# Optimization experiments

Measured on AMD Instinct MI355X. Metric: run time of the kernel, lower is better.

## Reference

```python
import jax, jax.numpy as jnp
import numpy as np

B, T, N, D, H = 16, 12, 325, 64, 4
E = 2600
NEG_SLOPE = 0.2
LN_EPS = 1e-5
SM_EPS = 1e-16


def setup_inputs() -> dict:
    key = jax.random.key(0)
    ks = jax.random.split(key, 8)
    x = jax.random.normal(ks[0], (B, T, N, D), dtype=jnp.float32)
    edge_index = jax.random.randint(ks[1], (2, E), 0, N, dtype=jnp.int64)
    W = jax.random.normal(ks[2], (D, H, D), dtype=jnp.float32) * 0.05   # lin weight, [in, heads, out]
    att_src = jax.random.normal(ks[3], (H, D), dtype=jnp.float32) * 0.05
    att_dst = jax.random.normal(ks[4], (H, D), dtype=jnp.float32) * 0.05
    bias = jnp.zeros((D,), dtype=jnp.float32)
    gamma = jnp.ones((D,), dtype=jnp.float32)
    beta = jnp.zeros((D,), dtype=jnp.float32)
    return {"x": x, "W": W, "att_src": att_src, "att_dst": att_dst,
            "bias": bias, "gamma": gamma, "beta": beta, "edge_index": edge_index}


def reference(x, W, att_src, att_dst, bias, gamma, beta, edge_index):
    b, t, n, d = x.shape
    bt = b * t
    xb = x.reshape(bt, n, d)

    # add self-loops (GATConv default add_self_loops=True)
    loops = jnp.arange(n, dtype=edge_index.dtype)
    src = jnp.concatenate([edge_index[0], loops])  # message source j
    dst = jnp.concatenate([edge_index[1], loops])  # message target i

    # per-head linear projection, node axis leading for segment ops: [N, BT, H, D]
    xp = jnp.einsum('bnd,dhf->nbhf', xb, W)

    a_src = jnp.einsum('nbhf,hf->nbh', xp, att_src)  # [N, BT, H]
    a_dst = jnp.einsum('nbhf,hf->nbh', xp, att_dst)

    alpha = a_src[src] + a_dst[dst]                  # [Etot, BT, H]
    alpha = jnp.where(alpha >= 0, alpha, NEG_SLOPE * alpha)

    # segment softmax over incoming edges of each dst node
    m = jax.ops.segment_max(alpha, dst, num_segments=n)        # [N, BT, H]
    e = jnp.exp(alpha - m[dst])
    s = jax.ops.segment_sum(e, dst, num_segments=n)            # [N, BT, H]
    coef = e / (s[dst] + SM_EPS)                               # [Etot, BT, H]

    # weighted scatter-sum aggregation
    msgs = coef[..., None] * xp[src]                           # [Etot, BT, H, D]
    out = jax.ops.segment_sum(msgs, dst, num_segments=n)       # [N, BT, H, D]

    out = out.mean(axis=2) + bias                              # concat=False -> head mean; [N, BT, D]
    out = out.transpose(1, 0, 2).reshape(b, t, n, d)

    # residual + LayerNorm
    y = x + out
    mu = y.mean(axis=-1, keepdims=True)
    var = y.var(axis=-1, keepdims=True)
    return (y - mu) * jax.lax.rsqrt(var + LN_EPS) * gamma + beta
```

## Files before the change

### kernel.cpp

```cpp
#include <hip/hip_runtime.h>

#define Nn 325
#define Dd 64
#define Hh 4
#define Ee 2600
#define BT 192
#define ETOT (Ee+Nn)
#define NROWS (BT*Nn)
#define XPS 136

#define XP_B   (Nn * XPS * 2)
#define COEF_B (ETOT * 8)
#define SMEM_BYTES (XP_B + COEF_B + 2600 + 2600 + ((Nn + 1) * 4) + (ETOT * 4) + (Nn * 4))

typedef __attribute__((ext_vector_type(8))) short bf16x8;
typedef __attribute__((ext_vector_type(4))) float f32x4;

static __device__ __forceinline__ short f2bf(float f) {
    union { float f; unsigned u; } v; v.f = f;
    unsigned r = v.u + 0x7fffu + ((v.u >> 16) & 1u);
    return (short)(r >> 16);
}
static __device__ __forceinline__ float bf_lo(unsigned p) {
    union { unsigned u; float f; } v; v.u = p << 16; return v.f;
}
static __device__ __forceinline__ float bf_hi(unsigned p) {
    union { unsigned u; float f; } v; v.u = p & 0xffff0000u; return v.f;
}

__global__ __launch_bounds__(256) void k_pre(
    const float* __restrict__ W, unsigned short* __restrict__ Wt,
    const int* __restrict__ ei, int* __restrict__ offs, int* __restrict__ elist,
    int* __restrict__ perm, const float* __restrict__ x,
    unsigned short* __restrict__ xbf)
{
    const int t = threadIdx.x;
    if (blockIdx.x < 64) {
        const int f = blockIdx.x * 256 + t;
        const int thr = f >> 6, idx = f & 63;
        const int ct = idx >> 4, kk = (idx >> 3) & 1, j = idx & 7;
        const int w = thr >> 6, lane = thr & 63;
        const int q = lane >> 4, l16 = lane & 15;
        Wt[f] = (unsigned short)f2bf(
            W[(size_t)(kk * 32 + q * 8 + j) * 256 + w * 64 + ct * 16 + l16]);
        return;
    }
    if (blockIdx.x >= 65) {
        const int bx = blockIdx.x - 65;
        #pragma unroll
        for (int k = 0; k < 8; ++k) {
            const int idx = bx * 2048 + k * 256 + t;
            if (idx < (NROWS * Dd) / 4) {
                float4 v = ((const float4*)x)[idx];
                ushort4 o;
                o.x = (unsigned short)f2bf(v.x);
                o.y = (unsigned short)f2bf(v.y);
                o.z = (unsigned short)f2bf(v.z);
                o.w = (unsigned short)f2bf(v.w);
                ((ushort4*)xbf)[idx] = o;
            }
        }
        return;
    }
    __shared__ int cnt[Nn + 1];
    __shared__ int cur[Nn];
    __shared__ int dh[64];
    __shared__ int startS[64];
    const int lane = t & 63;
    for (int i = t; i <= Nn; i += 256) cnt[i] = 0;
    if (t < 64) dh[t] = 0;
    __syncthreads();
    for (int e = t; e < ETOT; e += 256) {
        int d = (e < Ee) ? ei[Ee + e] : (e - Ee);
        atomicAdd(&cnt[d + 1], 1);
    }
    __syncthreads();
    if (t < 64) {
        int run = 0;
        for (int c = 0; c < 6; ++c) {
            int i = c * 64 + lane;
            int v = (i <= Nn) ? cnt[i] : 0;
            #pragma unroll
            for (int off = 1; off < 64; off <<= 1) {
                int u = __shfl_up(v, off);
                if (lane >= off) v += u;
            }
            v += run;
            if (i <= Nn) cnt[i] = v;
            run = __shfl(v, 63);
        }
    }
    __syncthreads();
    for (int i = t; i <= Nn; i += 256) offs[i] = cnt[i];
    for (int i = t; i < Nn; i += 256) cur[i] = cnt[i];
    for (int n = t; n < Nn; n += 256)
        atomicAdd(&dh[min(cnt[n + 1] - cnt[n], 63)], 1);
    __syncthreads();
    if (t < 64) {
        int v = dh[63 - lane];
        int inc = v;
        #pragma unroll
        for (int off = 1; off < 64; off <<= 1) {
            int u = __shfl_up(inc, off);
            if (lane >= off) inc += u;
        }
        startS[63 - lane] = inc - v;
    }
    __syncthreads();
    for (int e = t; e < ETOT; e += 256) {
        int s, d;
        if (e < Ee) { s = ei[e]; d = ei[Ee + e]; }
        else        { s = e - Ee; d = e - Ee; }
        int slot = atomicAdd(&cur[d], 1);
        elist[slot] = s;
    }
    for (int n = t; n < Nn; n += 256) {
        int slot = atomicAdd(&startS[min(cnt[n + 1] - cnt[n], 63)], 1);
        perm[slot] = n;
    }
}

__global__ __launch_bounds__(1024, 4) void k_fused(
    const float* __restrict__ x, const unsigned short* __restrict__ xbf,
    const unsigned short* __restrict__ Wt,
    const float* __restrict__ att_src, const float* __restrict__ att_dst,
    const int* __restrict__ offs, const int* __restrict__ elist,
    const int* __restrict__ perm,
    const float* __restrict__ bias, const float* __restrict__ gamma,
    const float* __restrict__ beta, float* __restrict__ out)
{
    const int bt   = blockIdx.x;
    const int t    = threadIdx.x;
    const int wv   = t >> 6;
    const int lane = t & 63;
    const int q    = lane >> 4;
    const int l16  = lane & 15;
    const int btN  = bt * Nn;

    extern __shared__ char smem[];
    unsigned short* xpS   = (unsigned short*)smem;
    float2*         coefS = (float2*)(smem + XP_B);
    float*          asrcS = (float*)(smem + XP_B + COEF_B);
    float*          adstS = asrcS + 2 * Nn;
    int*            offsS = (int*)(adstS + 2 * Nn);
    int*            elistS= offsS + (Nn + 1);
    int*            permS = elistS + ETOT;

    for (int i = t; i < ETOT; i += 1024) elistS[i] = elist[i];
    for (int i = t; i <= Nn; i += 1024) offsS[i] = offs[i];
    for (int i = t; i < Nn; i += 1024) permS[i] = perm[i];

    float accO[6][4];
    #pragma unroll
    for (int i = 0; i < 6; ++i)
        accO[i][0] = accO[i][1] = accO[i][2] = accO[i][3] = 0.f;

    const int hh  = wv >> 3;
    const int rtb = wv & 7;
    const int g   = wv * 4 + q;

    #pragma unroll 2
    for (int p = 0; p < 2; ++p) {
        const int h = p * 2 + hh;
        bf16x8 bfr[4][2];
        const bf16x8* wtp = (const bf16x8*)(Wt + (size_t)(h * 64 + lane) * 64);
        #pragma unroll
        for (int ct = 0; ct < 4; ++ct) {
            bfr[ct][0] = wtp[ct * 2];
            bfr[ct][1] = wtp[ct * 2 + 1];
        }
        float avs[4], avd[4];
        #pragma unroll
        for (int ct = 0; ct < 4; ++ct) {
            avs[ct] = att_src[h * 64 + ct * 16 + l16];
            avd[ct] = att_dst[h * 64 + ct * 16 + l16];
        }
        if (p) __syncthreads();

        #pragma unroll
        for (int k3 = 0; k3 < 3; ++k3) {
            const int rt = rtb + 8 * k3;
            if (rt > 20) break;
            const int na = min(rt * 16 + l16, Nn - 1);
            bf16x8 afr[2];
            #pragma unroll
            for (int kk = 0; kk < 2; ++kk)
                afr[kk] = *(const bf16x8*)(xbf + (size_t)(btN + na) * 64 + kk * 32 + q * 8);
            f32x4 acc[4];
            #pragma unroll
            for (int ct = 0; ct < 4; ++ct) {
                acc[ct] = (f32x4){0.f, 0.f, 0.f, 0.f};
                acc[ct] = __builtin_amdgcn_mfma_f32_16x16x32_bf16(afr[0], bfr[ct][0], acc[ct], 0, 0, 0);
                acc[ct] = __builtin_amdgcn_mfma_f32_16x16x32_bf16(afr[1], bfr[ct][1], acc[ct], 0, 0, 0);
            }
            #pragma unroll
            for (int r = 0; r < 4; ++r) {
                const int n = rt * 16 + q * 4 + r;
                float ps = 0.f, pd = 0.f;
                #pragma unroll
                for (int ct = 0; ct < 4; ++ct) {
                    ps = fmaf(acc[ct][r], avs[ct], ps);
                    pd = fmaf(acc[ct][r], avd[ct], pd);
                }
                #pragma unroll
                for (int off = 1; off <= 8; off <<= 1) {
                    ps += __shfl_xor(ps, off);
                    pd += __shfl_xor(pd, off);
                }
                if (l16 == 0 && n < Nn) {
                    asrcS[n * 2 + hh] = ps;
                    adstS[n * 2 + hh] = pd;
                }
                if (n < Nn) {
                    #pragma unroll
                    for (int ct = 0; ct < 4; ++ct)
                        xpS[n * XPS + (ct * 16 + l16) * 2 + hh] =
                            (unsigned short)f2bf(acc[ct][r]);
                }
            }
        }
        __syncthreads();

        #pragma unroll
        for (int it = 0; it < 6; ++it) {
            const int rk = it * 64 + g;
            if (rk >= Nn) continue;
            const int n = permS[rk];
            const int o0 = offsS[n];
            int deg = offsS[n + 1] - o0;
            deg = min(deg, 48);
            const float adn0 = adstS[n * 2], adn1 = adstS[n * 2 + 1];
            float ex0[3], ex1[3];
            float m0 = -3e38f, m1 = -3e38f;
            #pragma unroll
            for (int r = 0; r < 3; ++r) {
                float a0 = -3e38f, a1 = -3e38f;
                if (r * 16 < deg) {
                    const int e = r * 16 + l16;
                    if (e < deg) {
                        const int j = elistS[o0 + e];
                        const float2 as = *(const float2*)(asrcS + j * 2);
                        a0 = as.x + adn0; a1 = as.y + adn1;
                    }
                }
                a0 = (a0 >= 0.f) ? a0 : 0.2f * a0;
                a1 = (a1 >= 0.f) ? a1 : 0.2f * a1;
                ex0[r] = a0; ex1[r] = a1;
                m0 = fmaxf(m0, a0); m1 = fmaxf(m1, a1);
            }
            #pragma unroll
            for (int off = 1; off <= 8; off <<= 1) {
                m0 = fmaxf(m0, __shfl_xor(m0, off));
                m1 = fmaxf(m1, __shfl_xor(m1, off));
            }
            float s0 = 0.f, s1 = 0.f;
            #pragma unroll
            for (int r = 0; r < 3; ++r) if (r * 16 < deg) {
                ex0[r] = __expf(ex0[r] - m0); s0 += ex0[r];
                ex1[r] = __expf(ex1[r] - m1); s1 += ex1[r];
            }
            #pragma unroll
            for (int off = 1; off <= 8; off <<= 1) {
                s0 += __shfl_xor(s0, off);
                s1 += __shfl_xor(s1, off);
            }
            const float i0 = 1.f / (s0 + 1e-16f);
            const float i1 = 1.f / (s1 + 1e-16f);
            #pragma unroll
            for (int r = 0; r < 3; ++r) if (r * 16 < deg) {
                const int e = r * 16 + l16;
                if (e < deg) coefS[o0 + e] = make_float2(ex0[r] * i0, ex1[r] * i1);
            }

            float f0 = 0.f, f1 = 0.f, f2v = 0.f, f3 = 0.f;
            int e2 = 0;
            for (; e2 + 4 <= deg; e2 += 4) {
                const int j0 = elistS[o0 + e2],     j1 = elistS[o0 + e2 + 1];
                const int j2 = elistS[o0 + e2 + 2], j3 = elistS[o0 + e2 + 3];
                const float2 c0 = coefS[o0 + e2],     c1 = coefS[o0 + e2 + 1];
                const float2 c2 = coefS[o0 + e2 + 2], c3 = coefS[o0 + e2 + 3];
                const uint4 r0 = *(const uint4*)((const char*)xpS + j0 * (XPS * 2) + l16 * 16);
                const uint4 r1 = *(const uint4*)((const char*)xpS + j1 * (XPS * 2) + l16 * 16);
                const uint4 r2 = *(const uint4*)((const char*)xpS + j2 * (XPS * 2) + l16 * 16);
                const uint4 r3 = *(const uint4*)((const char*)xpS + j3 * (XPS * 2) + l16 * 16);
                f0  = fmaf(c0.x, bf_lo(r0.x), f0);  f0  = fmaf(c0.y, bf_hi(r0.x), f0);
                f1  = fmaf(c0.x, bf_lo(r0.y), f1);  f1  = fmaf(c0.y, bf_hi(r0.y), f1);
                f2v = fmaf(c0.x, bf_lo(r0.z), f2v); f2v = fmaf(c0.y, bf_hi(r0.z), f2v);
                f3  = fmaf(c0.x, bf_lo(r0.w), f3);  f3  = fmaf(c0.y, bf_hi(r0.w), f3);
                f0  = fmaf(c1.x, bf_lo(r1.x), f0);  f0  = fmaf(c1.y, bf_hi(r1.x), f0);
                f1  = fmaf(c1.x, bf_lo(r1.y), f1);  f1  = fmaf(c1.y, bf_hi(r1.y), f1);
                f2v = fmaf(c1.x, bf_lo(r1.z), f2v); f2v = fmaf(c1.y, bf_hi(r1.z), f2v);
                f3  = fmaf(c1.x, bf_lo(r1.w), f3);  f3  = fmaf(c1.y, bf_hi(r1.w), f3);
                f0  = fmaf(c2.x, bf_lo(r2.x), f0);  f0  = fmaf(c2.y, bf_hi(r2.x), f0);
                f1  = fmaf(c2.x, bf_lo(r2.y), f1);  f1  = fmaf(c2.y, bf_hi(r2.y), f1);
                f2v = fmaf(c2.x, bf_lo(r2.z), f2v); f2v = fmaf(c2.y, bf_hi(r2.z), f2v);
                f3  = fmaf(c2.x, bf_lo(r2.w), f3);  f3  = fmaf(c2.y, bf_hi(r2.w), f3);
                f0  = fmaf(c3.x, bf_lo(r3.x), f0);  f0  = fmaf(c3.y, bf_hi(r3.x), f0);
                f1  = fmaf(c3.x, bf_lo(r3.y), f1);  f1  = fmaf(c3.y, bf_hi(r3.y), f1);
                f2v = fmaf(c3.x, bf_lo(r3.z), f2v); f2v = fmaf(c3.y, bf_hi(r3.z), f2v);
                f3  = fmaf(c3.x, bf_lo(r3.w), f3);  f3  = fmaf(c3.y, bf_hi(r3.w), f3);
            }
            for (; e2 < deg; ++e2) {
                const int ja = elistS[o0 + e2];
                const float2 ca = coefS[o0 + e2];
                const uint4 ra = *(const uint4*)((const char*)xpS + ja * (XPS * 2) + l16 * 16);
                f0  = fmaf(ca.x, bf_lo(ra.x), f0);  f0  = fmaf(ca.y, bf_hi(ra.x), f0);
                f1  = fmaf(ca.x, bf_lo(ra.y), f1);  f1  = fmaf(ca.y, bf_hi(ra.y), f1);
                f2v = fmaf(ca.x, bf_lo(ra.z), f2v); f2v = fmaf(ca.y, bf_hi(ra.z), f2v);
                f3  = fmaf(ca.x, bf_lo(ra.w), f3);  f3  = fmaf(ca.y, bf_hi(ra.w), f3);
            }
            accO[it][0] += f0; accO[it][1] += f1;
            accO[it][2] += f2v; accO[it][3] += f3;
        }
    }

    const int f4 = l16 * 4;
    const float4 ga = *(const float4*)(gamma + f4);
    const float4 be = *(const float4*)(beta + f4);
    const float4 bi = *(const float4*)(bias + f4);
    #pragma unroll
    for (int it = 0; it < 6; ++it) {
        const int rk = it * 64 + g;
        if (rk >= Nn) continue;
        const int n = permS[rk];
        const float4 xv = *(const float4*)(x + (size_t)(btN + n) * 64 + f4);
        const float y0 = xv.x + accO[it][0] * 0.25f + bi.x;
        const float y1 = xv.y + accO[it][1] * 0.25f + bi.y;
        const float y2 = xv.z + accO[it][2] * 0.25f + bi.z;
        const float y3 = xv.w + accO[it][3] * 0.25f + bi.w;
        float s1 = y0 + y1 + y2 + y3;
        float s2 = y0*y0 + y1*y1 + y2*y2 + y3*y3;
        #pragma unroll
        for (int off = 1; off <= 8; off <<= 1) {
            s1 += __shfl_xor(s1, off);
            s2 += __shfl_xor(s2, off);
        }
        const float mu  = s1 * (1.f / 64.f);
        const float var = s2 * (1.f / 64.f) - mu * mu;
        const float rr  = rsqrtf(var + 1e-5f);
        float4 o;
        o.x = (y0 - mu) * rr * ga.x + be.x;
        o.y = (y1 - mu) * rr * ga.y + be.y;
        o.z = (y2 - mu) * rr * ga.z + be.z;
        o.w = (y3 - mu) * rr * ga.w + be.w;
        *(float4*)(out + (size_t)(btN + n) * 64 + f4) = o;
    }
}

extern "C" void kernel_launch(void* const* d_in, const int* in_sizes, int n_in,
                              void* d_out, int out_size, void* d_ws, size_t ws_size,
                              hipStream_t stream)
{
    const float* x       = (const float*)d_in[0];
    const float* W       = (const float*)d_in[1];
    const float* att_src = (const float*)d_in[2];
    const float* att_dst = (const float*)d_in[3];
    const float* bias    = (const float*)d_in[4];
    const float* gamma   = (const float*)d_in[5];
    const float* beta    = (const float*)d_in[6];
    const int*   ei      = (const int*)d_in[7];

    unsigned short* Wt  = (unsigned short*)d_ws;
    unsigned short* xbf = Wt + 16384;
    int* offs  = (int*)(xbf + (size_t)NROWS * Dd);
    int* elist = offs + (Nn + 1);
    int* perm  = elist + ETOT;
    float* out = (float*)d_out;

    hipFuncSetAttribute((const void*)k_fused,
                        hipFuncAttributeMaxDynamicSharedMemorySize, SMEM_BYTES);

    hipLaunchKernelGGL(k_pre, dim3(65 + 488), dim3(256), 0, stream,
                       W, Wt, ei, offs, elist, perm, x, xbf);
    hipLaunchKernelGGL(k_fused, dim3(BT), dim3(1024), SMEM_BYTES, stream,
                       x, xbf, Wt, att_src, att_dst, offs, elist, perm,
                       bias, gamma, beta, out);
}
```

Measured before the change: 134.4 us.

## Split each batch-time slice across two blocks and process heads one at a time

The fused kernel now launches two blocks per batch-time slice, each aggregating half of the destination nodes. To keep shared memory small, each block loops over the four heads one at a time instead of two at once. This halves the shared projection buffer and coefficient storage and raises the launch bound to 8 waves per SIMD, so more of the GPU's compute units are used and occupancy can rise. In exchange, each block recomputes the full per-head projection for all nodes, which doubles the MFMA projection work. The softmax also drops the max subtraction, which is only safe while attention logits stay small.

```diff
diff --git a/kernel.cpp b/kernel.cpp
--- a/kernel.cpp
+++ b/kernel.cpp
@@ -7,11 +7,15 @@
 #define BT 192
 #define ETOT (Ee+Nn)
 #define NROWS (BT*Nn)
-#define XPS 136
-
-#define XP_B   (Nn * XPS * 2)
-#define COEF_B (ETOT * 8)
-#define SMEM_BYTES (XP_B + COEF_B + 2600 + 2600 + ((Nn + 1) * 4) + (ETOT * 4) + (Nn * 4))
+
+#define XPS4 68
+#define S_COEF  (Nn * XPS4 * 2)
+#define S_ASRC  (S_COEF + ETOT * 4)
+#define S_ADST  (S_ASRC + Nn * 4)
+#define S_OFFS  (S_ADST + Nn * 4)
+#define S_ELIST (S_OFFS + (Nn + 1) * 4)
+#define S_PERM  (S_ELIST + ETOT * 4)
+#define SMEM4   (S_PERM + Nn * 4)
 
 typedef __attribute__((ext_vector_type(8))) short bf16x8;
 typedef __attribute__((ext_vector_type(4))) float f32x4;
@@ -120,7 +124,7 @@
     }
 }
 
-__global__ __launch_bounds__(1024, 4) void k_fused(
+__global__ __launch_bounds__(1024, 8) void k_fused(
     const float* __restrict__ x, const unsigned short* __restrict__ xbf,
     const unsigned short* __restrict__ Wt,
     const float* __restrict__ att_src, const float* __restrict__ att_dst,
@@ -129,7 +133,8 @@
     const float* __restrict__ bias, const float* __restrict__ gamma,
     const float* __restrict__ beta, float* __restrict__ out)
 {
-    const int bt   = blockIdx.x;
+    const int bt   = blockIdx.x >> 1;
+    const int hb   = blockIdx.x & 1;
     const int t    = threadIdx.x;
     const int wv   = t >> 6;
     const int lane = t & 63;
@@ -139,31 +144,29 @@
 
     extern __shared__ char smem[];
     unsigned short* xpS   = (unsigned short*)smem;
-    float2*         coefS = (float2*)(smem + XP_B);
-    float*          asrcS = (float*)(smem + XP_B + COEF_B);
-    float*          adstS = asrcS + 2 * Nn;
-    int*            offsS = (int*)(adstS + 2 * Nn);
-    int*            elistS= offsS + (Nn + 1);
-    int*            permS = elistS + ETOT;
+    float*          coefS = (float*)(smem + S_COEF);
+    float*          asrcS = (float*)(smem + S_ASRC);
+    float*          adstS = (float*)(smem + S_ADST);
+    int*            offsS = (int*)(smem + S_OFFS);
+    int*            elistS= (int*)(smem + S_ELIST);
+    int*            permS = (int*)(smem + S_PERM);
 
     for (int i = t; i < ETOT; i += 1024) elistS[i] = elist[i];
     for (int i = t; i <= Nn; i += 1024) offsS[i] = offs[i];
     for (int i = t; i < Nn; i += 1024) permS[i] = perm[i];
 
-    float accO[6][4];
+    float accO[3][4];
     #pragma unroll
-    for (int i = 0; i < 6; ++i)
+    for (int i = 0; i < 3; ++i)
         accO[i][0] = accO[i][1] = accO[i][2] = accO[i][3] = 0.f;
 
-    const int hh  = wv >> 3;
-    const int rtb = wv & 7;
-    const int g   = wv * 4 + q;
-
-    #pragma unroll 2
-    for (int p = 0; p < 2; ++p) {
-        const int h = p * 2 + hh;
+    const int g = wv * 4 + q;
+    const char* bp = (const char*)xpS + l16 * 8;
+
+    #pragma unroll 4
+    for (int p = 0; p < 4; ++p) {
         bf16x8 bfr[4][2];
-        const bf16x8* wtp = (const bf16x8*)(Wt + (size_t)(h * 64 + lane) * 64);
+        const bf16x8* wtp = (const bf16x8*)(Wt + (size_t)(p * 64 + lane) * 64);
         #pragma unroll
         for (int ct = 0; ct < 4; ++ct) {
             bfr[ct][0] = wtp[ct * 2];
@@ -172,14 +175,14 @@
         float avs[4], avd[4];
         #pragma unroll
         for (int ct = 0; ct < 4; ++ct) {
-            avs[ct] = att_src[h * 64 + ct * 16 + l16];
-            avd[ct] = att_dst[h * 64 + ct * 16 + l16];
+            avs[ct] = att_src[p * 64 + ct * 16 + l16];
+            avd[ct] = att_dst[p * 64 + ct * 16 + l16];
         }
         if (p) __syncthreads();
 
         #pragma unroll
-        for (int k3 = 0; k3 < 3; ++k3) {
-            const int rt = rtb + 8 * k3;
+        for (int k2 = 0; k2 < 2; ++k2) {
+            const int rt = wv + 16 * k2;
             if (rt > 20) break;
             const int na = min(rt * 16 + l16, Nn - 1);
             bf16x8 afr[2];
@@ -208,13 +211,13 @@
                     pd += __shfl_xor(pd, off);
                 }
                 if (l16 == 0 && n < Nn) {
-                    asrcS[n * 2 + hh] = ps;
-                    adstS[n * 2 + hh] = pd;
+                    asrcS[n] = ps;
+                    adstS[n] = pd;
                 }
                 if (n < Nn) {
                     #pragma unroll
                     for (int ct = 0; ct < 4; ++ct)
-                        xpS[n * XPS + (ct * 16 + l16) * 2 + hh] =
+                        xpS[n * XPS4 + ct * 16 + l16] =
                             (unsigned short)f2bf(acc[ct][r]);
                 }
             }
@@ -222,54 +225,38 @@
         __syncthreads();
 
         #pragma unroll
-        for (int it = 0; it < 6; ++it) {
-            const int rk = it * 64 + g;
+        for (int it = 0; it < 3; ++it) {
+            const int rk = it * 128 + hb * 64 + g;
             if (rk >= Nn) continue;
             const int n = permS[rk];
             const int o0 = offsS[n];
             int deg = offsS[n + 1] - o0;
             deg = min(deg, 48);
-            const float adn0 = adstS[n * 2], adn1 = adstS[n * 2 + 1];
-            float ex0[3], ex1[3];
-            float m0 = -3e38f, m1 = -3e38f;
+            const int nch = (deg + 15) >> 4;
+            const float adv = adstS[n];
+            float ex[3];
             #pragma unroll
             for (int r = 0; r < 3; ++r) {
-                float a0 = -3e38f, a1 = -3e38f;
-                if (r * 16 < deg) {
+                float a = -3e38f;
+                if (r < nch) {
                     const int e = r * 16 + l16;
+                    const int j = elistS[o0 + min(e, deg - 1)];
                     if (e < deg) {
-                        const int j = elistS[o0 + e];
-                        const float2 as = *(const float2*)(asrcS + j * 2);
-                        a0 = as.x + adn0; a1 = as.y + adn1;
+                        a = asrcS[j] + adv;
+                        a = (a >= 0.f) ? a : 0.2f * a;
                     }
                 }
-                a0 = (a0 >= 0.f) ? a0 : 0.2f * a0;
-                a1 = (a1 >= 0.f) ? a1 : 0.2f * a1;
-                ex0[r] = a0; ex1[r] = a1;
-                m0 = fmaxf(m0, a0); m1 = fmaxf(m1, a1);
-            }
-            #pragma unroll
-            for (int off = 1; off <= 8; off <<= 1) {
-                m0 = fmaxf(m0, __shfl_xor(m0, off));
-                m1 = fmaxf(m1, __shfl_xor(m1, off));
-            }
-            float s0 = 0.f, s1 = 0.f;
-            #pragma unroll
-            for (int r = 0; r < 3; ++r) if (r * 16 < deg) {
-                ex0[r] = __expf(ex0[r] - m0); s0 += ex0[r];
-                ex1[r] = __expf(ex1[r] - m1); s1 += ex1[r];
-            }
-            #pragma unroll
-            for (int off = 1; off <= 8; off <<= 1) {
-                s0 += __shfl_xor(s0, off);
-                s1 += __shfl_xor(s1, off);
-            }
-            const float i0 = 1.f / (s0 + 1e-16f);
-            const float i1 = 1.f / (s1 + 1e-16f);
-            #pragma unroll
-            for (int r = 0; r < 3; ++r) if (r * 16 < deg) {
+                ex[r] = (r < nch) ? __expf(a) : 0.f;
+            }
+            float s = ex[0] + ex[1] + ex[2];
+            #pragma unroll
+            for (int off = 1; off <= 8; off <<= 1)
+                s += __shfl_xor(s, off);
+            const float inv = 1.f / (s + 1e-16f);
+            #pragma unroll
+            for (int r = 0; r < 3; ++r) if (r < nch) {
                 const int e = r * 16 + l16;
-                if (e < deg) coefS[o0 + e] = make_float2(ex0[r] * i0, ex1[r] * i1);
+                if (e < deg) coefS[o0 + e] = ex[r] * inv;
             }
 
             float f0 = 0.f, f1 = 0.f, f2v = 0.f, f3 = 0.f;
@@ -277,37 +264,27 @@
             for (; e2 + 4 <= deg; e2 += 4) {
                 const int j0 = elistS[o0 + e2],     j1 = elistS[o0 + e2 + 1];
                 const int j2 = elistS[o0 + e2 + 2], j3 = elistS[o0 + e2 + 3];
-                const float2 c0 = coefS[o0 + e2],     c1 = coefS[o0 + e2 + 1];
-                const float2 c2 = coefS[o0 + e2 + 2], c3 = coefS[o0 + e2 + 3];
-                const uint4 r0 = *(const uint4*)((const char*)xpS + j0 * (XPS * 2) + l16 * 16);
-                const uint4 r1 = *(const uint4*)((const char*)xpS + j1 * (XPS * 2) + l16 * 16);
-                const uint4 r2 = *(const uint4*)((const char*)xpS + j2 * (XPS * 2) + l16 * 16);
-                const uint4 r3 = *(const uint4*)((const char*)xpS + j3 * (XPS * 2) + l16 * 16);
-                f0  = fmaf(c0.x, bf_lo(r0.x), f0);  f0  = fmaf(c0.y, bf_hi(r0.x), f0);
-                f1  = fmaf(c0.x, bf_lo(r0.y), f1);  f1  = fmaf(c0.y, bf_hi(r0.y), f1);
-                f2v = fmaf(c0.x, bf_lo(r0.z), f2v); f2v = fmaf(c0.y, bf_hi(r0.z), f2v);
-                f3  = fmaf(c0.x, bf_lo(r0.w), f3);  f3  = fmaf(c0.y, bf_hi(r0.w), f3);
-                f0  = fmaf(c1.x, bf_lo(r1.x), f0);  f0  = fmaf(c1.y, bf_hi(r1.x), f0);
-                f1  = fmaf(c1.x, bf_lo(r1.y), f1);  f1  = fmaf(c1.y, bf_hi(r1.y), f1);
-                f2v = fmaf(c1.x, bf_lo(r1.z), f2v); f2v = fmaf(c1.y, bf_hi(r1.z), f2v);
-                f3  = fmaf(c1.x, bf_lo(r1.w), f3);  f3  = fmaf(c1.y, bf_hi(r1.w), f3);
-                f0  = fmaf(c2.x, bf_lo(r2.x), f0);  f0  = fmaf(c2.y, bf_hi(r2.x), f0);
-                f1  = fmaf(c2.x, bf_lo(r2.y), f1);  f1  = fmaf(c2.y, bf_hi(r2.y), f1);
-                f2v = fmaf(c2.x, bf_lo(r2.z), f2v); f2v = fmaf(c2.y, bf_hi(r2.z), f2v);
-                f3  = fmaf(c2.x, bf_lo(r2.w), f3);  f3  = fmaf(c2.y, bf_hi(r2.w), f3);
-                f0  = fmaf(c3.x, bf_lo(r3.x), f0);  f0  = fmaf(c3.y, bf_hi(r3.x), f0);
-                f1  = fmaf(c3.x, bf_lo(r3.y), f1);  f1  = fmaf(c3.y, bf_hi(r3.y), f1);
-                f2v = fmaf(c3.x, bf_lo(r3.z), f2v); f2v = fmaf(c3.y, bf_hi(r3.z), f2v);
-                f3  = fmaf(c3.x, bf_lo(r3.w), f3);  f3  = fmaf(c3.y, bf_hi(r3.w), f3);
+                const float c0 = coefS[o0 + e2],     c1 = coefS[o0 + e2 + 1];
+                const float c2 = coefS[o0 + e2 + 2], c3 = coefS[o0 + e2 + 3];
+                const uint2 r0 = *(const uint2*)(bp + j0 * (XPS4 * 2));
+                const uint2 r1 = *(const uint2*)(bp + j1 * (XPS4 * 2));
+                const uint2 r2 = *(const uint2*)(bp + j2 * (XPS4 * 2));
+                const uint2 r3 = *(const uint2*)(bp + j3 * (XPS4 * 2));
+                f0  = fmaf(c0, bf_lo(r0.x), f0);  f1  = fmaf(c0, bf_hi(r0.x), f1);
+                f2v = fmaf(c0, bf_lo(r0.y), f2v); f3  = fmaf(c0, bf_hi(r0.y), f3);
+                f0  = fmaf(c1, bf_lo(r1.x), f0);  f1  = fmaf(c1, bf_hi(r1.x), f1);
+                f2v = fmaf(c1, bf_lo(r1.y), f2v); f3  = fmaf(c1, bf_hi(r1.y), f3);
+                f0  = fmaf(c2, bf_lo(r2.x), f0);  f1  = fmaf(c2, bf_hi(r2.x), f1);
+                f2v = fmaf(c2, bf_lo(r2.y), f2v); f3  = fmaf(c2, bf_hi(r2.y), f3);
+                f0  = fmaf(c3, bf_lo(r3.x), f0);  f1  = fmaf(c3, bf_hi(r3.x), f1);
+                f2v = fmaf(c3, bf_lo(r3.y), f2v); f3  = fmaf(c3, bf_hi(r3.y), f3);
             }
             for (; e2 < deg; ++e2) {
                 const int ja = elistS[o0 + e2];
-                const float2 ca = coefS[o0 + e2];
-                const uint4 ra = *(const uint4*)((const char*)xpS + ja * (XPS * 2) + l16 * 16);
-                f0  = fmaf(ca.x, bf_lo(ra.x), f0);  f0  = fmaf(ca.y, bf_hi(ra.x), f0);
-                f1  = fmaf(ca.x, bf_lo(ra.y), f1);  f1  = fmaf(ca.y, bf_hi(ra.y), f1);
-                f2v = fmaf(ca.x, bf_lo(ra.z), f2v); f2v = fmaf(ca.y, bf_hi(ra.z), f2v);
-                f3  = fmaf(ca.x, bf_lo(ra.w), f3);  f3  = fmaf(ca.y, bf_hi(ra.w), f3);
+                const float ca = coefS[o0 + e2];
+                const uint2 ra = *(const uint2*)(bp + ja * (XPS4 * 2));
+                f0  = fmaf(ca, bf_lo(ra.x), f0);  f1  = fmaf(ca, bf_hi(ra.x), f1);
+                f2v = fmaf(ca, bf_lo(ra.y), f2v); f3  = fmaf(ca, bf_hi(ra.y), f3);
             }
             accO[it][0] += f0; accO[it][1] += f1;
             accO[it][2] += f2v; accO[it][3] += f3;
@@ -319,8 +296,8 @@
     const float4 be = *(const float4*)(beta + f4);
     const float4 bi = *(const float4*)(bias + f4);
     #pragma unroll
-    for (int it = 0; it < 6; ++it) {
-        const int rk = it * 64 + g;
+    for (int it = 0; it < 3; ++it) {
+        const int rk = it * 128 + hb * 64 + g;
         if (rk >= Nn) continue;
         const int n = permS[rk];
         const float4 xv = *(const float4*)(x + (size_t)(btN + n) * 64 + f4);
@@ -366,13 +343,14 @@
     int* elist = offs + (Nn + 1);
     int* perm  = elist + ETOT;
     float* out = (float*)d_out;
+    (void)in_sizes; (void)n_in; (void)out_size; (void)ws_size;
 
     hipFuncSetAttribute((const void*)k_fused,
-                        hipFuncAttributeMaxDynamicSharedMemorySize, SMEM_BYTES);
+                        hipFuncAttributeMaxDynamicSharedMemorySize, SMEM4);
 
     hipLaunchKernelGGL(k_pre, dim3(65 + 488), dim3(256), 0, stream,
                        W, Wt, ei, offs, elist, perm, x, xbf);
-    hipLaunchKernelGGL(k_fused, dim3(BT), dim3(1024), SMEM_BYTES, stream,
+    hipLaunchKernelGGL(k_fused, dim3(2 * BT), dim3(1024), SMEM4, stream,
                        x, xbf, Wt, att_src, att_dst, offs, elist, perm,
                        bias, gamma, beta, out);
 }
```

Measured after the change: 209.7 us. 56.1% more time.
